# Kernel tuning notes

Hardware: AMD Instinct MI355X
Metric: run time of the kernel (lower is better)

Reference implementation:

```python
import jax, jax.numpy as jnp
import numpy as np

B, S, D = 2, 512, 256

def setup_inputs() -> dict:
    key = jax.random.key(0)
    k1, k2, k3, k4, k5 = jax.random.split(key, 5)
    return {
        "query": jax.random.normal(k1, (B, S, D), dtype=jnp.float32),
        "key": jax.random.normal(k2, (B, S, D), dtype=jnp.float32),
        "value": jax.random.normal(k3, (B, S, D), dtype=jnp.float32),
        "Wm_w": jax.random.normal(k4, (D, D), dtype=jnp.float32) * (1.0 / np.sqrt(D)),
        "vm_w": jax.random.normal(k5, (1, D), dtype=jnp.float32) * (1.0 / np.sqrt(D)),
    }

def reference(query, key, value, Wm_w, vm_w):
    # pairwise difference: q.unsqueeze(1) - q.unsqueeze(2) -> [B, S, S, D]
    diff = query[:, None, :, :] - query[:, :, None, :]
    # Wm (Linear, no bias): [B,S,S,D] @ Wm_w^T, then tanh
    h = jnp.tanh(jnp.einsum('bijd,ed->bije', diff, Wm_w))
    # vm (Linear D->1, no bias) + squeeze -> scores [B, S, S]
    sjt = jnp.einsum('bije,e->bij', h, vm_w[0])
    # softmax over dim=2 (eval mode: dropout is identity)
    atten = jax.nn.softmax(sjt, axis=2)
    # bmm(atten, value) -> [B, S, D]
    context = jnp.einsum('bij,bjd->bid', atten, value)
    return context, atten
```

## Files before the change

### kernel.cpp

```cpp
#include <hip/hip_runtime.h>

#define B 2
#define S 512
#define D 256
#define C2L 2.885390081777927f
#define LOG2E 1.4426950408889634f

__global__ __launch_bounds__(256) void proj_kernel(const float* __restrict__ q,
                                                   const float* __restrict__ W,
                                                   float* __restrict__ EJ,
                                                   float* __restrict__ EN) {
    __shared__ float qlds[4 * D];
    const int t = threadIdx.x;
    const int b = blockIdx.x / (S / 4);
    const int i0 = (blockIdx.x % (S / 4)) * 4;
    const float* qbase = q + (size_t)(b * S + i0) * D;
    for (int idx = t; idx < 4 * D; idx += 256) qlds[idx] = qbase[idx];
    __syncthreads();
    const float* wr = W + (size_t)t * D;
    float a0 = 0.f, a1 = 0.f, a2 = 0.f, a3 = 0.f;
#pragma unroll 4
    for (int d = 0; d < D; ++d) {
        float w = wr[d];
        a0 = fmaf(qlds[d], w, a0);
        a1 = fmaf(qlds[D + d], w, a1);
        a2 = fmaf(qlds[2 * D + d], w, a2);
        a3 = fmaf(qlds[3 * D + d], w, a3);
    }
    a0 *= C2L; a1 *= C2L; a2 *= C2L; a3 *= C2L;
    float* ej = EJ + (size_t)(b * D + t) * S + i0;
    *(float4*)ej = make_float4(__builtin_amdgcn_exp2f(a0), __builtin_amdgcn_exp2f(a1),
                               __builtin_amdgcn_exp2f(a2), __builtin_amdgcn_exp2f(a3));
    EN[(size_t)(b * S + i0 + 0) * D + t] = __builtin_amdgcn_exp2f(-a0);
    EN[(size_t)(b * S + i0 + 1) * D + t] = __builtin_amdgcn_exp2f(-a1);
    EN[(size_t)(b * S + i0 + 2) * D + t] = __builtin_amdgcn_exp2f(-a2);
    EN[(size_t)(b * S + i0 + 3) * D + t] = __builtin_amdgcn_exp2f(-a3);
}

__global__ __launch_bounds__(512) void fused_kernel(const float* __restrict__ EJ,
                                                    const float* __restrict__ EN,
                                                    const float* __restrict__ vm,
                                                    const float* __restrict__ value,
                                                    float* __restrict__ att,
                                                    float* __restrict__ ctx) {
    __shared__ float en2[D][2];
    __shared__ float wl[D];
    __shared__ float a2s[S][2];
    __shared__ float part[2][8][64][4];
    __shared__ float redm[2][8], reds[2][8];

    const int t = threadIdx.x;
    const int b = blockIdx.x >> 8;
    const int i0 = (blockIdx.x & 255) * 2;

    if (t < D) wl[t] = -2.f * vm[t];
    {
        const int e = t & 255, r = t >> 8;
        en2[e][r] = EN[((size_t)(b * S + i0 + r)) * D + e];
    }
    __syncthreads();

    float acc0 = 0.f, acc1 = 0.f;
    const float* ejp = EJ + (size_t)b * D * S + t;
#pragma unroll 8
    for (int e = 0; e < D; ++e) {
        float ev = ejp[(size_t)e * S];
        float w = wl[e];
        float2 f = *(const float2*)&en2[e][0];
        float y0 = fmaf(ev, f.x, 1.f);
        float y1 = fmaf(ev, f.y, 1.f);
        float r0 = __builtin_amdgcn_rcpf(y0);
        float r1 = __uint_as_float(0x7EF311C3u - __float_as_uint(y1));
        r1 = r1 * fmaf(-y1, r1, 2.f);
        r1 = r1 * fmaf(-y1, r1, 2.f);
        acc0 = fmaf(w, r0, acc0);
        acc1 = fmaf(w, r1, acc1);
    }

    const int lane = t & 63, wv = t >> 6;
    {
        float lm0 = acc0, lm1 = acc1;
#pragma unroll
        for (int off = 32; off; off >>= 1) {
            lm0 = fmaxf(lm0, __shfl_xor(lm0, off));
            lm1 = fmaxf(lm1, __shfl_xor(lm1, off));
        }
        if (lane == 0) { redm[0][wv] = lm0; redm[1][wv] = lm1; }
    }
    __syncthreads();
    float m0 = redm[0][0], m1 = redm[1][0];
#pragma unroll
    for (int w = 1; w < 8; ++w) {
        m0 = fmaxf(m0, redm[0][w]);
        m1 = fmaxf(m1, redm[1][w]);
    }
    float p0 = __builtin_amdgcn_exp2f((acc0 - m0) * LOG2E);
    float p1 = __builtin_amdgcn_exp2f((acc1 - m1) * LOG2E);
    {
        float ls0 = p0, ls1 = p1;
#pragma unroll
        for (int off = 32; off; off >>= 1) {
            ls0 += __shfl_xor(ls0, off);
            ls1 += __shfl_xor(ls1, off);
        }
        if (lane == 0) { reds[0][wv] = ls0; reds[1][wv] = ls1; }
    }
    __syncthreads();
    float s0 = 0.f, s1 = 0.f;
#pragma unroll
    for (int w = 0; w < 8; ++w) { s0 += reds[0][w]; s1 += reds[1][w]; }
    float a0 = p0 * __builtin_amdgcn_rcpf(s0);
    float a1 = p1 * __builtin_amdgcn_rcpf(s1);
    a2s[t][0] = a0;
    a2s[t][1] = a1;
    att[(size_t)(b * S + i0) * S + t] = a0;
    att[(size_t)(b * S + i0 + 1) * S + t] = a1;
    __syncthreads();

    {
        const int dq = t & 63, js = t >> 6;
        float4 c0 = {}, c1 = {};
        const float* vb = value + (size_t)b * S * D + (size_t)dq * 4;
#pragma unroll 4
        for (int jj = 0; jj < 64; ++jj) {
            int j = js * 64 + jj;
            float4 v = *(const float4*)(vb + (size_t)j * D);
            float w0 = a2s[j][0], w1 = a2s[j][1];
            c0.x = fmaf(w0, v.x, c0.x); c0.y = fmaf(w0, v.y, c0.y);
            c0.z = fmaf(w0, v.z, c0.z); c0.w = fmaf(w0, v.w, c0.w);
            c1.x = fmaf(w1, v.x, c1.x); c1.y = fmaf(w1, v.y, c1.y);
            c1.z = fmaf(w1, v.z, c1.z); c1.w = fmaf(w1, v.w, c1.w);
        }
        *(float4*)&part[0][js][dq][0] = c0;
        *(float4*)&part[1][js][dq][0] = c1;
    }
    __syncthreads();
    if (t < 128) {
        const int row = t >> 6, dq = t & 63;
        float4 sum = {};
#pragma unroll
        for (int js = 0; js < 8; ++js) {
            float4 pt = *(const float4*)&part[row][js][dq][0];
            sum.x += pt.x; sum.y += pt.y; sum.z += pt.z; sum.w += pt.w;
        }
        *(float4*)(ctx + (size_t)(b * S + i0 + row) * D + (size_t)dq * 4) = sum;
    }
}

extern "C" void kernel_launch(void* const* d_in, const int* in_sizes, int n_in,
                              void* d_out, int out_size, void* d_ws, size_t ws_size,
                              hipStream_t stream) {
    const float* q = (const float*)d_in[0];
    const float* value = (const float*)d_in[2];
    const float* W = (const float*)d_in[3];
    const float* vm = (const float*)d_in[4];

    float* ctx = (float*)d_out;
    float* att = ctx + (size_t)B * S * D;
    float* EJ = (float*)d_ws;
    float* EN = EJ + (size_t)B * D * S;

    proj_kernel<<<B * (S / 4), 256, 0, stream>>>(q, W, EJ, EN);
    fused_kernel<<<B * (S / 2), 512, 0, stream>>>(EJ, EN, vm, value, att, ctx);
}
```

Before: 49.60 us.

## Share one reciprocal across two rows and interleave EJ layout for float4 loads

Rewrites the inner tanh-sum loop so both query rows share one hardware reciprocal of y0*y1, replacing the separate rcp and the Newton-iteration reciprocal. The EJ intermediate is stored interleaved in groups of four features, so each thread loads a float4 per step. EN rows and the scaled vm weights are now read directly from global memory (precomputed by the projection kernel) instead of being staged in LDS. The launch bound also asks for two blocks per CU. Risks include overflow or precision loss when forming the product y0*y1, and extra global/L1 traffic for the broadcast EN and weight loads.

```diff
diff --git a/kernel.cpp b/kernel.cpp
--- a/kernel.cpp
+++ b/kernel.cpp
@@ -8,12 +8,15 @@
 
 __global__ __launch_bounds__(256) void proj_kernel(const float* __restrict__ q,
                                                    const float* __restrict__ W,
-                                                   float* __restrict__ EJ,
-                                                   float* __restrict__ EN) {
+                                                   const float* __restrict__ vm,
+                                                   float* __restrict__ EJ4,
+                                                   float* __restrict__ EN,
+                                                   float* __restrict__ W2) {
     __shared__ float qlds[4 * D];
     const int t = threadIdx.x;
     const int b = blockIdx.x / (S / 4);
     const int i0 = (blockIdx.x % (S / 4)) * 4;
+    if (blockIdx.x == 0) W2[t] = -2.f * vm[t];
     const float* qbase = q + (size_t)(b * S + i0) * D;
     for (int idx = t; idx < 4 * D; idx += 256) qlds[idx] = qbase[idx];
     __syncthreads();
@@ -28,23 +31,23 @@
         a3 = fmaf(qlds[3 * D + d], w, a3);
     }
     a0 *= C2L; a1 *= C2L; a2 *= C2L; a3 *= C2L;
-    float* ej = EJ + (size_t)(b * D + t) * S + i0;
-    *(float4*)ej = make_float4(__builtin_amdgcn_exp2f(a0), __builtin_amdgcn_exp2f(a1),
-                               __builtin_amdgcn_exp2f(a2), __builtin_amdgcn_exp2f(a3));
+    float* ejb = EJ4 + (((size_t)(b * 64 + (t >> 2))) * S + i0) * 4 + (t & 3);
+    ejb[0]  = __builtin_amdgcn_exp2f(a0);
+    ejb[4]  = __builtin_amdgcn_exp2f(a1);
+    ejb[8]  = __builtin_amdgcn_exp2f(a2);
+    ejb[12] = __builtin_amdgcn_exp2f(a3);
     EN[(size_t)(b * S + i0 + 0) * D + t] = __builtin_amdgcn_exp2f(-a0);
     EN[(size_t)(b * S + i0 + 1) * D + t] = __builtin_amdgcn_exp2f(-a1);
     EN[(size_t)(b * S + i0 + 2) * D + t] = __builtin_amdgcn_exp2f(-a2);
     EN[(size_t)(b * S + i0 + 3) * D + t] = __builtin_amdgcn_exp2f(-a3);
 }
 
-__global__ __launch_bounds__(512) void fused_kernel(const float* __restrict__ EJ,
-                                                    const float* __restrict__ EN,
-                                                    const float* __restrict__ vm,
-                                                    const float* __restrict__ value,
-                                                    float* __restrict__ att,
-                                                    float* __restrict__ ctx) {
-    __shared__ float en2[D][2];
-    __shared__ float wl[D];
+__global__ __launch_bounds__(512, 2) void fused_kernel(const float* __restrict__ EJ4,
+                                                       const float* __restrict__ EN,
+                                                       const float* __restrict__ W2,
+                                                       const float* __restrict__ value,
+                                                       float* __restrict__ att,
+                                                       float* __restrict__ ctx) {
     __shared__ float a2s[S][2];
     __shared__ float part[2][8][64][4];
     __shared__ float redm[2][8], reds[2][8];
@@ -53,31 +56,37 @@
     const int b = blockIdx.x >> 8;
     const int i0 = (blockIdx.x & 255) * 2;
 
-    if (t < D) wl[t] = -2.f * vm[t];
-    {
-        const int e = t & 255, r = t >> 8;
-        en2[e][r] = EN[((size_t)(b * S + i0 + r)) * D + e];
-    }
-    __syncthreads();
+    const float4* ejp = (const float4*)EJ4 + (size_t)b * 64 * S + t;
+    const float4* f0p = (const float4*)(EN + ((size_t)(b * S + i0)) * D);
+    const float4* f1p = (const float4*)(EN + ((size_t)(b * S + i0 + 1)) * D);
+    const float4* wp  = (const float4*)W2;
 
     float acc0 = 0.f, acc1 = 0.f;
-    const float* ejp = EJ + (size_t)b * D * S + t;
-#pragma unroll 8
-    for (int e = 0; e < D; ++e) {
-        float ev = ejp[(size_t)e * S];
-        float w = wl[e];
-        float2 f = *(const float2*)&en2[e][0];
-        float y0 = fmaf(ev, f.x, 1.f);
-        float y1 = fmaf(ev, f.y, 1.f);
-        float r0 = __builtin_amdgcn_rcpf(y0);
-        float r1 = __uint_as_float(0x7EF311C3u - __float_as_uint(y1));
-        r1 = r1 * fmaf(-y1, r1, 2.f);
-        r1 = r1 * fmaf(-y1, r1, 2.f);
-        acc0 = fmaf(w, r0, acc0);
-        acc1 = fmaf(w, r1, acc1);
+#pragma unroll 4
+    for (int g = 0; g < 64; ++g) {
+        float4 ev4 = ejp[(size_t)g * S];
+        float4 f0 = f0p[g];
+        float4 f1 = f1p[g];
+        float4 wv = wp[g];
+#pragma unroll
+        for (int c = 0; c < 4; ++c) {
+            const float ev = (c == 0) ? ev4.x : (c == 1) ? ev4.y
+                           : (c == 2) ? ev4.z : ev4.w;
+            const float fa = (c == 0) ? f0.x : (c == 1) ? f0.y
+                           : (c == 2) ? f0.z : f0.w;
+            const float fb = (c == 0) ? f1.x : (c == 1) ? f1.y
+                           : (c == 2) ? f1.z : f1.w;
+            const float w  = (c == 0) ? wv.x : (c == 1) ? wv.y
+                           : (c == 2) ? wv.z : wv.w;
+            float y0 = fmaf(ev, fa, 1.f);
+            float y1 = fmaf(ev, fb, 1.f);
+            float r  = __builtin_amdgcn_rcpf(y0 * y1);
+            acc0 = fmaf(w * y1, r, acc0);
+            acc1 = fmaf(w * y0, r, acc1);
+        }
     }
 
-    const int lane = t & 63, wv = t >> 6;
+    const int lane = t & 63, wv8 = t >> 6;
     {
         float lm0 = acc0, lm1 = acc1;
 #pragma unroll
@@ -85,7 +94,7 @@
             lm0 = fmaxf(lm0, __shfl_xor(lm0, off));
             lm1 = fmaxf(lm1, __shfl_xor(lm1, off));
         }
-        if (lane == 0) { redm[0][wv] = lm0; redm[1][wv] = lm1; }
+        if (lane == 0) { redm[0][wv8] = lm0; redm[1][wv8] = lm1; }
     }
     __syncthreads();
     float m0 = redm[0][0], m1 = redm[1][0];
@@ -103,7 +112,7 @@
             ls0 += __shfl_xor(ls0, off);
             ls1 += __shfl_xor(ls1, off);
         }
-        if (lane == 0) { reds[0][wv] = ls0; reds[1][wv] = ls1; }
+        if (lane == 0) { reds[0][wv8] = ls0; reds[1][wv8] = ls1; }
     }
     __syncthreads();
     float s0 = 0.f, s1 = 0.f;
@@ -123,9 +132,9 @@
         const float* vb = value + (size_t)b * S * D + (size_t)dq * 4;
 #pragma unroll 4
         for (int jj = 0; jj < 64; ++jj) {
-            int j = js * 64 + jj;
-            float4 v = *(const float4*)(vb + (size_t)j * D);
-            float w0 = a2s[j][0], w1 = a2s[j][1];
+            int jx = js * 64 + jj;
+            float4 v = *(const float4*)(vb + (size_t)jx * D);
+            float w0 = a2s[jx][0], w1 = a2s[jx][1];
             c0.x = fmaf(w0, v.x, c0.x); c0.y = fmaf(w0, v.y, c0.y);
             c0.z = fmaf(w0, v.z, c0.z); c0.w = fmaf(w0, v.w, c0.w);
             c1.x = fmaf(w1, v.x, c1.x); c1.y = fmaf(w1, v.y, c1.y);
@@ -157,9 +166,10 @@
 
     float* ctx = (float*)d_out;
     float* att = ctx + (size_t)B * S * D;
-    float* EJ = (float*)d_ws;
-    float* EN = EJ + (size_t)B * D * S;
+    float* EJ4 = (float*)d_ws;
+    float* EN = EJ4 + (size_t)B * D * S;
+    float* W2 = EN + (size_t)B * S * D;
 
-    proj_kernel<<<B * (S / 4), 256, 0, stream>>>(q, W, EJ, EN);
-    fused_kernel<<<B * (S / 2), 512, 0, stream>>>(EJ, EN, vm, value, att, ctx);
+    proj_kernel<<<B * (S / 4), 256, 0, stream>>>(q, W, vm, EJ4, EN, W2);
+    fused_kernel<<<B * (S / 2), 512, 0, stream>>>(EJ4, EN, W2, value, att, ctx);
 }
```

Result: faster. 42.49 us (-14.3%).
